# Kernel optimization log

Measured on AMD Instinct MI355X. Metric: run time of the kernel, lower is better.

## Reference

```python
import jax, jax.numpy as jnp
import numpy as np

B, TDEC, V, T1, T2 = 8, 256, 16000, 256, 256
VOOV = V + 256  # vocab_size_oov
NEG = -1e20


def _make_onehot(idx, T):
    # mimic get_one_hot_input: OOV positions map to V + t, col 0 zeroed
    pos = jnp.arange(T)[None, :]
    mapped = jnp.where(idx < V, idx, V + pos)
    oh = jax.nn.one_hot(mapped, V + T, dtype=jnp.float32)
    return oh.at[:, :, 0].set(0.0)


def setup_inputs() -> dict:
    key = jax.random.key(0)
    k = jax.random.split(key, 5)
    gen_score = jax.random.normal(k[0], (B, TDEC, V), jnp.float32)
    cp_score1 = jax.random.normal(k[1], (B, TDEC, T1), jnp.float32)
    cp_score2 = jax.random.normal(k[2], (B, TDEC, T2), jnp.float32)
    idx_oov1 = jax.random.randint(k[3], (B, T1), 0, VOOV)
    idx_oov2 = jax.random.randint(k[4], (B, T2), 0, VOOV)
    onehot1 = _make_onehot(idx_oov1, T1)
    onehot2 = _make_onehot(idx_oov2, T2)
    return {"gen_score": gen_score, "cp_score1": cp_score1, "cp_score2": cp_score2,
            "onehot1": onehot1, "onehot2": onehot2,
            "idx_oov1": idx_oov1, "idx_oov2": idx_oov2, "vocab_size_oov": VOOV}


def _scatter_lse(cp, idx, v, n_oov):
    # cp: [B,Tdec,T] log-probs; idx: [B,T]; reduce duplicates with logsumexp
    Tdec = cp.shape[1]
    safe = jnp.where(idx >= v, idx - v, n_oov)  # non-OOV -> trash bucket n_oov

    def scat(cp_b, s_b):
        return jnp.zeros((Tdec, n_oov + 1), cp.dtype).at[:, s_b].add(jnp.exp(cp_b))

    return jax.vmap(scat)(cp, safe)  # [B,Tdec,n_oov+1] accumulated exp-sums


def reference(gen_score, cp_score1, cp_score2, onehot1, onehot2,
              idx_oov1, idx_oov2, vocab_size_oov):
    v = gen_score.shape[2]
    n_oov = vocab_size_oov - v
    # project copy scores into extended-vocab columns (einsum 'imj,ijn->imn')
    cps1 = jnp.einsum('btj,bjn->btn', cp_score1, onehot1)  # [B,Tdec,V+T1]
    cps2 = jnp.einsum('btj,bjn->btn', cp_score2, onehot2)  # [B,Tdec,V+T2]
    norm = jax.nn.log_softmax(jnp.concatenate([gen_score, cps1, cps2], axis=2), axis=2)
    w1 = onehot1.shape[2]
    gen = norm[:, :, :v]
    blk1 = norm[:, :, v:v + w1]
    blk2 = norm[:, :, v + w1:]
    # in-vocab copy mass merges with gen via logsumexp
    gen_final = jax.scipy.special.logsumexp(
        jnp.stack([gen, blk1[:, :, :v], blk2[:, :, :v]], axis=3), axis=3)
    # OOV copy mass: scatter-logsumexp over duplicate indices, init -1e20
    acc = _scatter_lse(blk1[:, :, v:], idx_oov1, v, n_oov)
    acc = acc + _scatter_lse(blk2[:, :, v:], idx_oov2, v, n_oov)
    s = acc[:, :, :n_oov]
    oov = jnp.where(s > 0, jnp.log(jnp.where(s > 0, s, 1.0)), NEG)
    return jnp.concatenate([gen_final, oov], axis=2)  # [B,Tdec,Voov]
```

## Files before the change

kernel.cpp:

```cpp
#include <hip/hip_runtime.h>
#include <hip/hip_bf16.h>
#include <math.h>

#define BQ     8
#define TDEC   256
#define NROWS  (BQ * TDEC)
#define VV     16000
#define TJ     256
#define NOOV   256
#define WOUT   (VV + NOOV)
#define NEGV   (-1e20f)
#define NV4    (VV / 4)
#define HSZ    512
#define NT     1024
#define NW     (NT / 64)

typedef float f32x4 __attribute__((ext_vector_type(4)));

__device__ __forceinline__ unsigned hstart(int n) {
    return ((unsigned)n * 2654435761u) >> 23;
}

__global__ __launch_bounds__(NT) void fused_kernel(
    const float* __restrict__ gen,
    const float* __restrict__ cp1,
    const float* __restrict__ cp2,
    const int*   __restrict__ idx1,
    const int*   __restrict__ idx2,
    float* __restrict__ out)
{
    __shared__ f32x4 dense4[NV4];
    __shared__ int   hkey[2 * HSZ];
    __shared__ float hval[2 * HSZ];
    __shared__ float oovacc[NOOV];
    __shared__ float redz[NW];
    float* dense = (float*)dense4;

    const int row = blockIdx.x;
    const int b   = row >> 8;
    const int tid = threadIdx.x;

    int   myidx = -1;
    float myval = 0.f;
    if (tid < 2 * TJ) {
        const int s = tid >> 8;
        const int j = tid & (TJ - 1);
        myidx = s ? idx2[b * TJ + j]          : idx1[b * TJ + j];
        myval = s ? cp2[(size_t)row * TJ + j] : cp1[(size_t)row * TJ + j];
    }

    const f32x4* grow4 = (const f32x4*)(gen + (size_t)row * VV);
    f32x4 v[4];
#pragma unroll
    for (int k = 0; k < 4; ++k) {
        const int f  = k * NT + tid;
        const int fc = (f < NV4) ? f : (NV4 - 1);
        v[k] = grow4[fc];
    }

    hkey[tid] = -1;
    hval[tid] = 0.f;
    if (tid < NOOV) oovacc[tid] = 0.f;
    __syncthreads();

    float z = 0.f;
    if (myidx > 0 && myidx < VV) {
        const int s = tid >> 8;
        int*   keys = hkey + s * HSZ;
        float* vals = hval + s * HSZ;
        unsigned h = hstart(myidx);
        for (;;) {
            const int prev = atomicCAS(&keys[h], -1, myidx);
            if (prev == -1 || prev == myidx) { atomicAdd(&vals[h], myval); break; }
            h = (h + 1) & (HSZ - 1);
        }
    } else if (myidx >= VV) {
        const float e = __expf(myval);
        z += e - 1.f;
        atomicAdd(&oovacc[myidx - VV], e);
    }
    __syncthreads();

    const int sk  = hkey[tid];
    float     inc = 0.f;
    if (sk >= 0) {
        inc = __expf(hval[tid]) - 1.f;
        z  += inc;
    }

#pragma unroll
    for (int k = 0; k < 4; ++k) {
        const int f = k * NT + tid;
        f32x4 e;
        e.x = __expf(v[k].x);
        e.y = __expf(v[k].y);
        e.z = __expf(v[k].z);
        e.w = __expf(v[k].w);
        if (f < NV4) {
            dense4[f] = e;
            z += (e.x + e.y) + (e.z + e.w);
        }
    }
    __syncthreads();

    if (sk >= 0) atomicAdd(&dense[sk], inc);

#pragma unroll
    for (int o = 32; o > 0; o >>= 1) z += __shfl_down(z, o, 64);
    if ((tid & 63) == 0) redz[tid >> 6] = z;
    __syncthreads();
    float zt = 2.f * (float)(VV + TJ);
#pragma unroll
    for (int w = 0; w < NW; ++w) zt += redz[w];
    const float logZ = __logf(zt);

    float* orow = out + (size_t)row * WOUT;

    if (tid < NOOV) {
        const float a = oovacc[tid];
        __builtin_nontemporal_store((a > 0.f) ? (__logf(a) - logZ) : NEGV,
                                    orow + VV + tid);
    }

#pragma unroll
    for (int k = 0; k < 4; ++k) {
        const int f = k * NT + tid;
        if (f < NV4) {
            const f32x4 d = dense4[f];
            f32x4 o;
            o.x = __logf(d.x + 2.f) - logZ;
            o.y = __logf(d.y + 2.f) - logZ;
            o.z = __logf(d.z + 2.f) - logZ;
            o.w = __logf(d.w + 2.f) - logZ;
            __builtin_nontemporal_store(o, (f32x4*)(orow + (size_t)f * 4));
        }
    }
}

extern "C" void kernel_launch(void* const* d_in, const int* in_sizes, int n_in,
                              void* d_out, int out_size, void* d_ws, size_t ws_size,
                              hipStream_t stream) {
    const float* gen  = (const float*)d_in[0];
    const float* cp1  = (const float*)d_in[1];
    const float* cp2  = (const float*)d_in[2];
    const int*   idx1 = (const int*)d_in[5];
    const int*   idx2 = (const int*)d_in[6];
    float* out = (float*)d_out;

    hipLaunchKernelGGL(fused_kernel, dim3(NROWS), dim3(NT), 0, stream,
                       gen, cp1, cp2, idx1, idx2, out);
}
```

Before: 48.89 us.

## Process two decoder rows per block, sharing the hash table and prefetching

Each block now handles two consecutive rows of the same batch item instead of one, and the grid is halved. The hash table of in-vocab copy indices is built once and serves both rows, with separate value accumulators per row. The second row's gen scores are loaded while the first row's outputs are being written, to overlap that load with the stores. The cost is more registers and LDS per block, fewer blocks in the grid, and a longer serial chain per block in a kernel that is already close to memory-bandwidth bound.

```diff
diff --git a/kernel.cpp b/kernel.cpp
--- a/kernel.cpp
+++ b/kernel.cpp
@@ -21,7 +21,7 @@
     return ((unsigned)n * 2654435761u) >> 23;
 }
 
-__global__ __launch_bounds__(NT) void fused_kernel(
+__global__ __launch_bounds__(NT) void fused2_kernel(
     const float* __restrict__ gen,
     const float* __restrict__ cp1,
     const float* __restrict__ cp2,
@@ -31,108 +31,160 @@
 {
     __shared__ f32x4 dense4[NV4];
     __shared__ int   hkey[2 * HSZ];
-    __shared__ float hval[2 * HSZ];
-    __shared__ float oovacc[NOOV];
+    __shared__ float hvalA[2 * HSZ];
+    __shared__ float hvalB[2 * HSZ];
+    __shared__ float oovA[NOOV];
+    __shared__ float oovB[NOOV];
     __shared__ float redz[NW];
     float* dense = (float*)dense4;
 
-    const int row = blockIdx.x;
-    const int b   = row >> 8;
-    const int tid = threadIdx.x;
+    const int pair = blockIdx.x;
+    const int rowA = pair * 2;
+    const int rowB = rowA + 1;
+    const int b    = rowA >> 8;
+    const int tid  = threadIdx.x;
 
     int   myidx = -1;
-    float myval = 0.f;
+    float vA = 0.f, vB = 0.f;
     if (tid < 2 * TJ) {
         const int s = tid >> 8;
         const int j = tid & (TJ - 1);
-        myidx = s ? idx2[b * TJ + j]          : idx1[b * TJ + j];
-        myval = s ? cp2[(size_t)row * TJ + j] : cp1[(size_t)row * TJ + j];
-    }
-
-    const f32x4* grow4 = (const f32x4*)(gen + (size_t)row * VV);
-    f32x4 v[4];
+        myidx = s ? idx2[b * TJ + j] : idx1[b * TJ + j];
+        const float* cp = s ? cp2 : cp1;
+        vA = cp[(size_t)rowA * TJ + j];
+        vB = cp[(size_t)rowB * TJ + j];
+    }
+
+    const f32x4* gA4 = (const f32x4*)(gen + (size_t)rowA * VV);
+    f32x4 va[4];
 #pragma unroll
     for (int k = 0; k < 4; ++k) {
         const int f  = k * NT + tid;
         const int fc = (f < NV4) ? f : (NV4 - 1);
-        v[k] = grow4[fc];
-    }
-
-    hkey[tid] = -1;
-    hval[tid] = 0.f;
-    if (tid < NOOV) oovacc[tid] = 0.f;
-    __syncthreads();
-
-    float z = 0.f;
+        va[k] = gA4[fc];
+    }
+
+    hkey[tid]  = -1;
+    hvalA[tid] = 0.f;
+    hvalB[tid] = 0.f;
+    if (tid < NOOV) { oovA[tid] = 0.f; oovB[tid] = 0.f; }
+    __syncthreads();
+
+    float zA = 0.f, zB = 0.f;
     if (myidx > 0 && myidx < VV) {
         const int s = tid >> 8;
-        int*   keys = hkey + s * HSZ;
-        float* vals = hval + s * HSZ;
+        int* keys = hkey + s * HSZ;
         unsigned h = hstart(myidx);
         for (;;) {
             const int prev = atomicCAS(&keys[h], -1, myidx);
-            if (prev == -1 || prev == myidx) { atomicAdd(&vals[h], myval); break; }
+            if (prev == -1 || prev == myidx) {
+                atomicAdd(&hvalA[s * HSZ + h], vA);
+                atomicAdd(&hvalB[s * HSZ + h], vB);
+                break;
+            }
             h = (h + 1) & (HSZ - 1);
         }
     } else if (myidx >= VV) {
-        const float e = __expf(myval);
-        z += e - 1.f;
-        atomicAdd(&oovacc[myidx - VV], e);
-    }
-    __syncthreads();
-
-    const int sk  = hkey[tid];
-    float     inc = 0.f;
+        const float eA = __expf(vA), eB = __expf(vB);
+        zA += eA - 1.f; zB += eB - 1.f;
+        atomicAdd(&oovA[myidx - VV], eA);
+        atomicAdd(&oovB[myidx - VV], eB);
+    }
+    __syncthreads();
+
+    const int sk = hkey[tid];
+    float incA = 0.f, incB = 0.f;
     if (sk >= 0) {
-        inc = __expf(hval[tid]) - 1.f;
-        z  += inc;
+        incA = __expf(hvalA[tid]) - 1.f;  zA += incA;
+        incB = __expf(hvalB[tid]) - 1.f;  zB += incB;
     }
 
 #pragma unroll
     for (int k = 0; k < 4; ++k) {
         const int f = k * NT + tid;
         f32x4 e;
-        e.x = __expf(v[k].x);
-        e.y = __expf(v[k].y);
-        e.z = __expf(v[k].z);
-        e.w = __expf(v[k].w);
-        if (f < NV4) {
-            dense4[f] = e;
-            z += (e.x + e.y) + (e.z + e.w);
-        }
-    }
-    __syncthreads();
-
-    if (sk >= 0) atomicAdd(&dense[sk], inc);
-
-#pragma unroll
-    for (int o = 32; o > 0; o >>= 1) z += __shfl_down(z, o, 64);
-    if ((tid & 63) == 0) redz[tid >> 6] = z;
-    __syncthreads();
-    float zt = 2.f * (float)(VV + TJ);
-#pragma unroll
-    for (int w = 0; w < NW; ++w) zt += redz[w];
-    const float logZ = __logf(zt);
-
-    float* orow = out + (size_t)row * WOUT;
-
+        e.x = __expf(va[k].x); e.y = __expf(va[k].y);
+        e.z = __expf(va[k].z); e.w = __expf(va[k].w);
+        if (f < NV4) { dense4[f] = e; zA += (e.x + e.y) + (e.z + e.w); }
+    }
+    __syncthreads();
+
+    if (sk >= 0) atomicAdd(&dense[sk], incA);
+#pragma unroll
+    for (int o = 32; o > 0; o >>= 1) zA += __shfl_down(zA, o, 64);
+    if ((tid & 63) == 0) redz[tid >> 6] = zA;
+    __syncthreads();
+    float ztA = 2.f * (float)(VV + TJ);
+#pragma unroll
+    for (int w = 0; w < NW; ++w) ztA += redz[w];
+    const float logZA = __logf(ztA);
+
+    const f32x4* gB4 = (const f32x4*)(gen + (size_t)rowB * VV);
+    f32x4 vb[4];
+#pragma unroll
+    for (int k = 0; k < 4; ++k) {
+        const int f  = k * NT + tid;
+        const int fc = (f < NV4) ? f : (NV4 - 1);
+        vb[k] = gB4[fc];
+    }
+
+    float* oA = out + (size_t)rowA * WOUT;
     if (tid < NOOV) {
-        const float a = oovacc[tid];
-        __builtin_nontemporal_store((a > 0.f) ? (__logf(a) - logZ) : NEGV,
-                                    orow + VV + tid);
-    }
-
+        const float a = oovA[tid];
+        __builtin_nontemporal_store((a > 0.f) ? (__logf(a) - logZA) : NEGV,
+                                    oA + VV + tid);
+    }
 #pragma unroll
     for (int k = 0; k < 4; ++k) {
         const int f = k * NT + tid;
         if (f < NV4) {
             const f32x4 d = dense4[f];
             f32x4 o;
-            o.x = __logf(d.x + 2.f) - logZ;
-            o.y = __logf(d.y + 2.f) - logZ;
-            o.z = __logf(d.z + 2.f) - logZ;
-            o.w = __logf(d.w + 2.f) - logZ;
-            __builtin_nontemporal_store(o, (f32x4*)(orow + (size_t)f * 4));
+            o.x = __logf(d.x + 2.f) - logZA;
+            o.y = __logf(d.y + 2.f) - logZA;
+            o.z = __logf(d.z + 2.f) - logZA;
+            o.w = __logf(d.w + 2.f) - logZA;
+            __builtin_nontemporal_store(o, (f32x4*)(oA + (size_t)f * 4));
+        }
+    }
+
+#pragma unroll
+    for (int k = 0; k < 4; ++k) {
+        const int f = k * NT + tid;
+        f32x4 e;
+        e.x = __expf(vb[k].x); e.y = __expf(vb[k].y);
+        e.z = __expf(vb[k].z); e.w = __expf(vb[k].w);
+        if (f < NV4) { dense4[f] = e; zB += (e.x + e.y) + (e.z + e.w); }
+    }
+    __syncthreads();
+
+    if (sk >= 0) atomicAdd(&dense[sk], incB);
+#pragma unroll
+    for (int o = 32; o > 0; o >>= 1) zB += __shfl_down(zB, o, 64);
+    if ((tid & 63) == 0) redz[tid >> 6] = zB;
+    __syncthreads();
+    float ztB = 2.f * (float)(VV + TJ);
+#pragma unroll
+    for (int w = 0; w < NW; ++w) ztB += redz[w];
+    const float logZB = __logf(ztB);
+
+    float* oB = out + (size_t)rowB * WOUT;
+    if (tid < NOOV) {
+        const float a = oovB[tid];
+        __builtin_nontemporal_store((a > 0.f) ? (__logf(a) - logZB) : NEGV,
+                                    oB + VV + tid);
+    }
+#pragma unroll
+    for (int k = 0; k < 4; ++k) {
+        const int f = k * NT + tid;
+        if (f < NV4) {
+            const f32x4 d = dense4[f];
+            f32x4 o;
+            o.x = __logf(d.x + 2.f) - logZB;
+            o.y = __logf(d.y + 2.f) - logZB;
+            o.z = __logf(d.z + 2.f) - logZB;
+            o.w = __logf(d.w + 2.f) - logZB;
+            __builtin_nontemporal_store(o, (f32x4*)(oB + (size_t)f * 4));
         }
     }
 }
@@ -147,6 +199,6 @@
     const int*   idx2 = (const int*)d_in[6];
     float* out = (float*)d_out;
 
-    hipLaunchKernelGGL(fused_kernel, dim3(NROWS), dim3(NT), 0, stream,
+    hipLaunchKernelGGL(fused2_kernel, dim3(NROWS / 2), dim3(NT), 0, stream,
                        gen, cp1, cp2, idx1, idx2, out);
 }
```

Result: faster. 46.99 us (-3.9%).
